# Kernel optimization log

Hardware: AMD Instinct MI355X
Metric: run time of the kernel (lower is better)

Reference implementation:

```python
import jax, jax.numpy as jnp
import numpy as np

NSAMPLE = 16
LEAKY = 0.1


def _leaky(x):
    return jnp.where(x >= 0, x, LEAKY * x)


def _sqdist(src, dst):
    # src [B,N,3], dst [B,M,3] -> [B,N,M]
    d = -2.0 * jnp.einsum('bnc,bmc->bnm', src, dst)
    d = d + jnp.sum(src * src, -1)[:, :, None]
    d = d + jnp.sum(dst * dst, -1)[:, None, :]
    return d


def _knn_idx(query, points, k):
    # query [B,N,3], points [B,M,3] -> [B,N,k] indices of k nearest points
    dist = _sqdist(query, points)
    _, idx = jax.lax.top_k(-dist, k)
    return idx


def _group(points, idx):
    # points [B,M,C], idx [B,N,K] -> [B,N,K,C]
    return jax.vmap(lambda p, i: p[i])(points, idx)


def _cross(xyz1, xyz2, p1, p2, pos_w, pos_b, mlp_params):
    # xyz1 [B,N1,3], xyz2 [B,N2,3], p1 [B,N1,C], p2 [B,N2,C]
    idx = _knn_idx(xyz1, xyz2, NSAMPLE)                       # [B,N1,K]
    neigh_xyz = _group(xyz2, idx)                             # [B,N1,K,3]
    direction = neigh_xyz - xyz1[:, :, None, :]               # [B,N1,K,3]
    g2 = _group(p2, idx)                                      # [B,N1,K,C]
    pos_feat = jnp.einsum('bnkc,oc->bnko', direction, pos_w) + pos_b
    new_pts = _leaky(g2 + p1[:, :, None, :] + pos_feat)       # [B,N1,K,C0]
    for w, b in mlp_params:
        new_pts = _leaky(jnp.einsum('bnkc,oc->bnko', new_pts, w) + b)
    return jnp.max(new_pts, axis=2)                           # [B,N1,Cl]


def setup_inputs() -> dict:
    key = jax.random.key(0)
    ks = jax.random.split(key, 14)
    B, N, D = 2, 8192, 64
    s = 0.1
    return {
        'pc1': jax.random.normal(ks[0], (B, N, 3), jnp.float32),
        'pc2': jax.random.normal(ks[1], (B, N, 3), jnp.float32),
        'feat1': jax.random.normal(ks[2], (B, N, D), jnp.float32),
        'feat2': jax.random.normal(ks[3], (B, N, D), jnp.float32),
        'pos_w': jax.random.normal(ks[4], (64, 3), jnp.float32) * s,
        'pos_b': jax.random.normal(ks[5], (64,), jnp.float32) * s,
        'mlp_w0': jax.random.normal(ks[6], (64, 64), jnp.float32) * s,
        'mlp_b0': jax.random.normal(ks[7], (64,), jnp.float32) * s,
        'mlp_w1': jax.random.normal(ks[8], (64, 64), jnp.float32) * s,
        'mlp_b1': jax.random.normal(ks[9], (64,), jnp.float32) * s,
        't1_w': jax.random.normal(ks[10], (128, 64), jnp.float32) * s,
        't1_b': jax.random.normal(ks[11], (128,), jnp.float32) * s,
        't2_w': jax.random.normal(ks[12], (128, 64), jnp.float32) * s,
        't2_b': jax.random.normal(ks[13], (128,), jnp.float32) * s,
    }


def reference(pc1, pc2, feat1, feat2, pos_w, pos_b, mlp_w0, mlp_b0,
              mlp_w1, mlp_b1, t1_w, t1_b, t2_w, t2_b):
    mlp = [(mlp_w0, mlp_b0), (mlp_w1, mlp_b1)]
    f1 = _cross(pc1, pc2, feat1, feat2, pos_w, pos_b, mlp)    # [B,N1,64]
    f1 = jnp.einsum('bnc,oc->bno', f1, t1_w) + t1_b           # [B,N1,128]
    f2 = _cross(pc2, pc1, feat2, feat1, pos_w, pos_b, mlp)
    f2 = jnp.einsum('bnc,oc->bno', f2, t2_w) + t2_b
    return f1, f2
```

## Files before the change

kernel.cpp:

```cpp
#include <hip/hip_runtime.h>

#define NPTS 8192
#define KNNK 16
#define NSLOT 17
#define LEAKY 0.1f

typedef short bf16x8 __attribute__((ext_vector_type(8)));
typedef float f32x4  __attribute__((ext_vector_type(4)));

#define KTH   1024
#define QPB   128
#define CHN   32
#define GQ    4
#define BUFCAP 48
#define LCAP  6144

__global__ __launch_bounds__(KTH, 4) void knn_kernel(
    const float* __restrict__ pc1, const float* __restrict__ pc2,
    int* __restrict__ knn_out)
{
    __shared__ float sx[NPTS], sy[NPTS], sz[NPTS];
    __shared__ float sbuf[QPB][2 * BUFCAP];
    __shared__ float sthr[QPB];
    __shared__ int   scnt[QPB];
    __shared__ float4 qcoef[QPB];
    __shared__ unsigned short list[LCAP];
    __shared__ int   lcnt;

    const int t   = threadIdx.x;
    const int q0  = blockIdx.x * QPB;
    const int dir = q0 >> 14;
    const int b   = (q0 >> 13) & 1;

    const float* __restrict__ pq    = dir ? pc2 : pc1;
    const float* __restrict__ pcand = dir ? pc1 : pc2;
    const int n0 = q0 & (NPTS - 1);

    const float* src = pcand + (size_t)b * NPTS * 3;
    for (int i = t; i < NPTS; i += KTH) {
        sx[i] = src[3 * i];
        sy[i] = src[3 * i + 1];
        sz[i] = src[3 * i + 2];
    }
    if (t < QPB) {
        scnt[t] = 0;
        const float* qp = pq + ((size_t)b * NPTS + n0 + t) * 3;
        qcoef[t] = make_float4(-2.0f * qp[0], -2.0f * qp[1], -2.0f * qp[2], 0.f);
    }
    if (t == 0) lcnt = 0;
    __syncthreads();

    const int ch = t & (CHN - 1);
    const int qg = t >> 5;

    float q2x[GQ], q2y[GQ], q2z[GQ];
    #pragma unroll
    for (int g = 0; g < GQ; ++g) {
        const float* qp = pq + ((size_t)b * NPTS + n0 + qg * GQ + g) * 3;
        q2x[g] = -2.0f * qp[0];
        q2y[g] = -2.0f * qp[1];
        q2z[g] = -2.0f * qp[2];
    }

    float mA[GQ], mB[GQ];
    #pragma unroll
    for (int g = 0; g < GQ; ++g) { mA[g] = 3.0e38f; mB[g] = 3.0e38f; }

    #pragma unroll 2
    for (int j = 0; j < 32; ++j) {
        const int i0 = j * 128 + 4 * ch;
        const int i1 = i0 + 4096;
        const f32x4 ax = *(const f32x4*)&sx[i0];
        const f32x4 ay = *(const f32x4*)&sy[i0];
        const f32x4 az = *(const f32x4*)&sz[i0];
        const f32x4 bx = *(const f32x4*)&sx[i1];
        const f32x4 by = *(const f32x4*)&sy[i1];
        const f32x4 bz = *(const f32x4*)&sz[i1];
        f32x4 an, bn;
        #pragma unroll
        for (int c = 0; c < 4; ++c) {
            an[c] = fmaf(ax[c], ax[c], fmaf(ay[c], ay[c], az[c] * az[c]));
            bn[c] = fmaf(bx[c], bx[c], fmaf(by[c], by[c], bz[c] * bz[c]));
        }
        #pragma unroll
        for (int g = 0; g < GQ; ++g) {
            #pragma unroll
            for (int c = 0; c < 4; ++c) {
                const float da = fmaf(q2x[g], ax[c],
                                 fmaf(q2y[g], ay[c],
                                 fmaf(q2z[g], az[c], an[c])));
                mA[g] = fminf(mA[g], da);
                const float db = fmaf(q2x[g], bx[c],
                                 fmaf(q2y[g], by[c],
                                 fmaf(q2z[g], bz[c], bn[c])));
                mB[g] = fminf(mB[g], db);
            }
        }
    }

    #pragma unroll
    for (int g = 0; g < GQ; ++g) {
        const int row = qg * GQ + g;
        sbuf[row][ch]      = mA[g];
        sbuf[row][32 + ch] = mB[g];
    }
    __builtin_amdgcn_wave_barrier();

    #pragma unroll
    for (int g = 0; g < GQ; ++g) {
        const int row = qg * GQ + g;
        const float vA = mA[g], vB = mB[g];
        int ltA = 0, eqA = 0, ltB = 0, eqB = 0;
        #pragma unroll
        for (int c = 0; c < 64; c += 2) {
            const float2 vp = *(const float2*)&sbuf[row][c];
            ltA += (vp.x < vA) ? 1 : 0;  eqA += (vp.x == vA) ? 1 : 0;
            ltA += (vp.y < vA) ? 1 : 0;  eqA += (vp.y == vA) ? 1 : 0;
            ltB += (vp.x < vB) ? 1 : 0;  eqB += (vp.x == vB) ? 1 : 0;
            ltB += (vp.y < vB) ? 1 : 0;  eqB += (vp.y == vB) ? 1 : 0;
        }
        if (ltA <= 16 && ltA + eqA > 16) sthr[row] = vA;
        if (ltB <= 16 && ltB + eqB > 16) sthr[row] = vB;
    }
    __syncthreads();

    #pragma unroll
    for (int g = 0; g < GQ; ++g) {
        const int row = qg * GQ + g;
        const float tqv = sthr[row];
        if (mA[g] <= tqv) {
            const int p = atomicAdd(&lcnt, 1);
            if (p < LCAP) list[p] = (unsigned short)((row << 6) | ch);
        }
        if (mB[g] <= tqv) {
            const int p = atomicAdd(&lcnt, 1);
            if (p < LCAP) list[p] = (unsigned short)((row << 6) | 32 | ch);
        }
    }
    __syncthreads();

    {
        const int nsub = min(lcnt, LCAP) * 8;
        for (int k = t; k < nsub; k += KTH) {
            const int e  = list[k >> 3];
            const int s  = k & 7;
            const int q  = e >> 6;
            const int hf = (e >> 5) & 1;
            const int cc = e & 31;
            const float4 qc = qcoef[q];
            const float tqv = sthr[q];
            #pragma unroll
            for (int jj = 0; jj < 4; ++jj) {
                const int i0 = hf * 4096 + (s * 4 + jj) * 128 + 4 * cc;
                const f32x4 cx = *(const f32x4*)&sx[i0];
                const f32x4 cy = *(const f32x4*)&sy[i0];
                const f32x4 cz = *(const f32x4*)&sz[i0];
                #pragma unroll
                for (int c = 0; c < 4; ++c) {
                    const float cn = fmaf(cx[c], cx[c],
                                     fmaf(cy[c], cy[c], cz[c] * cz[c]));
                    const float d  = fmaf(qc.x, cx[c],
                                     fmaf(qc.y, cy[c],
                                     fmaf(qc.z, cz[c], cn)));
                    if (d <= tqv) {
                        const int pos = atomicAdd(&scnt[q], 1);
                        if (pos < BUFCAP) {
                            sbuf[q][pos] = d;
                            ((int*)&sbuf[q][BUFCAP])[pos] = i0 + c;
                        }
                    }
                }
            }
        }
    }
    __syncthreads();

    if (t < QPB) {
        const int nc = min(scnt[t], BUFCAP);

        float dist[NSLOT];
        int   ind[NSLOT];
        #pragma unroll
        for (int i = 0; i < NSLOT; ++i) { dist[i] = 3.0e38f; ind[i] = 0x7fffffff; }

        for (int s = 0; s < nc; ++s) {
            const float d  = sbuf[t][s];
            const int   id = ((int*)&sbuf[t][BUFCAP])[s];
            const bool better0 = (d < dist[0]) || (d == dist[0] && id < ind[0]);
            if (better0) {
                bool cprev = true;
                #pragma unroll
                for (int i = 0; i < NSLOT - 1; ++i) {
                    const bool ci = (d < dist[i + 1]) ||
                                    (d == dist[i + 1] && id < ind[i + 1]);
                    const float nv = ci ? dist[i + 1] : (cprev ? d  : dist[i]);
                    const int   ni = ci ? ind[i + 1]  : (cprev ? id : ind[i]);
                    dist[i] = nv; ind[i] = ni;
                    cprev = ci;
                }
                if (cprev) { dist[NSLOT - 1] = d; ind[NSLOT - 1] = id; }
            }
        }

        const float* qpp = pq + ((size_t)b * NPTS + n0 + t) * 3;
        const double dqx = (double)qpp[0], dqy = (double)qpp[1], dqz = (double)qpp[2];
        double dd[NSLOT];
        #pragma unroll
        for (int i = 0; i < NSLOT; ++i) {
            const int id = ind[i];
            const double dx = (double)sx[id] - dqx;
            const double dy = (double)sy[id] - dqy;
            const double dz = (double)sz[id] - dqz;
            dd[i] = dx * dx + dy * dy + dz * dz;
        }
        int worst = 0; double wd = dd[0];
        #pragma unroll
        for (int i = 1; i < NSLOT; ++i) { if (dd[i] > wd) { wd = dd[i]; worst = i; } }

        int* outp = knn_out + (size_t)(q0 + t) * KNNK;
        int slot = 0;
        #pragma unroll
        for (int i = 0; i < NSLOT; ++i) {
            if (i != worst) outp[slot++] = ind[i];
        }
    }
}

#define PTS 16
#define NG  4

__device__ __forceinline__ unsigned int packhl(float f) {
    const unsigned int u = __float_as_uint(f);
    const unsigned int h = u & 0xffff0000u;
    const float lf = f - __uint_as_float(h);
    return h | (__float_as_uint(lf) >> 16);
}

__device__ __forceinline__ void build_b(const float* __restrict__ wrow,
                                        bf16x8* hi, bf16x8* lo) {
    union { unsigned int u[4]; bf16x8 v; } H, L;
    #pragma unroll
    for (int r = 0; r < 4; ++r) {
        const float f0 = wrow[2 * r], f1 = wrow[2 * r + 1];
        const unsigned int h0 = __float_as_uint(f0) & 0xffff0000u;
        const unsigned int h1 = __float_as_uint(f1) & 0xffff0000u;
        const float l0 = f0 - __uint_as_float(h0);
        const float l1 = f1 - __uint_as_float(h1);
        H.u[r] = h1 | (h0 >> 16);
        L.u[r] = (__float_as_uint(l1) & 0xffff0000u) | (__float_as_uint(l0) >> 16);
    }
    *hi = H.v; *lo = L.v;
}

__device__ __forceinline__ void unpack_a(const unsigned int* __restrict__ Tu,
                                         bf16x8* hi, bf16x8* lo) {
    union { unsigned int u[4]; bf16x8 v; } H, L;
    #pragma unroll
    for (int r = 0; r < 4; ++r) {
        const unsigned int a = Tu[2 * r + 1], bb = Tu[2 * r];
        H.u[r] = __builtin_amdgcn_perm(a, bb, 0x07060302u);
        L.u[r] = __builtin_amdgcn_perm(a, bb, 0x05040100u);
    }
    *hi = H.v; *lo = L.v;
}

__device__ __forceinline__ f32x4 mfma3(f32x4 acc, bf16x8 ah, bf16x8 al,
                                       bf16x8 bh, bf16x8 bl) {
    acc = __builtin_amdgcn_mfma_f32_16x16x32_bf16(ah, bl, acc, 0, 0, 0);
    acc = __builtin_amdgcn_mfma_f32_16x16x32_bf16(al, bh, acc, 0, 0, 0);
    acc = __builtin_amdgcn_mfma_f32_16x16x32_bf16(ah, bh, acc, 0, 0, 0);
    return acc;
}

__global__ __launch_bounds__(256, 4) void feat_kernel(
    const float* __restrict__ pc1, const float* __restrict__ pc2,
    const float* __restrict__ feat1, const float* __restrict__ feat2,
    const float* __restrict__ pos_w, const float* __restrict__ pos_b,
    const float* __restrict__ w0, const float* __restrict__ b0,
    const float* __restrict__ w1, const float* __restrict__ b1,
    const float* __restrict__ t1w, const float* __restrict__ t1b,
    const float* __restrict__ t2w, const float* __restrict__ t2b,
    const int* __restrict__ knn, float* __restrict__ out)
{
    __shared__ unsigned int T0[4][16][68];
    __shared__ unsigned int T1[4][16][68];
    __shared__ float sm[PTS][64];

    const int t    = threadIdx.x;
    const int w    = t >> 6;
    const int lane = t & 63;
    const int m    = lane & 15;
    const int quad = lane >> 4;

    const int p0  = blockIdx.x * PTS;
    const int dir = p0 >> 14, bt = (p0 >> 13) & 1;
    const int n0  = p0 & (NPTS - 1);

    const float* __restrict__ pqd = dir ? pc2 : pc1;
    const float* __restrict__ pcd = dir ? pc1 : pc2;
    const float* __restrict__ fqd = dir ? feat2 : feat1;
    const float* __restrict__ fcd = dir ? feat1 : feat2;

    const int ocol = w * 16 + m;
    bf16x8 Bh[2][2], Bl[2][2];
    #pragma unroll
    for (int kt = 0; kt < 2; ++kt) {
        build_b(&w0[(size_t)ocol * 64 + kt * 32 + quad * 8], &Bh[0][kt], &Bl[0][kt]);
        build_b(&w1[(size_t)ocol * 64 + kt * 32 + quad * 8], &Bh[1][kt], &Bl[1][kt]);
    }
    const float bias1 = b0[ocol];
    const float bias2 = b1[ocol];

    const int cg0 = w * 16 + quad * 4;
    float pbc[4], pwx[4], pwy[4], pwz[4];
    #pragma unroll
    for (int i = 0; i < 4; ++i) {
        pbc[i] = pos_b[cg0 + i];
        pwx[i] = pos_w[(cg0 + i) * 3 + 0];
        pwy[i] = pos_w[(cg0 + i) * 3 + 1];
        pwz[i] = pos_w[(cg0 + i) * 3 + 2];
    }

    float  sdx[4], sdy[4], sdz[4];
    float4 sgf[4], sfq[4];

    auto loadg = [&](int gg) {
        #pragma unroll
        for (int pt = 0; pt < 4; ++pt) {
            const int pp = p0 + gg * 4 + pt;
            const int nn = n0 + gg * 4 + pt;
            const int id = knn[(size_t)pp * KNNK + m];
            const float* qp  = pqd + ((size_t)bt * NPTS + nn) * 3;
            const float* nbp = pcd + ((size_t)bt * NPTS + id) * 3;
            sdx[pt] = nbp[0] - qp[0];
            sdy[pt] = nbp[1] - qp[1];
            sdz[pt] = nbp[2] - qp[2];
            sgf[pt] = *(const float4*)&fcd[((size_t)bt * NPTS + id) * 64 + cg0];
            sfq[pt] = *(const float4*)&fqd[((size_t)bt * NPTS + nn) * 64 + cg0];
        }
    };

    auto storeg = [&]() {
        #pragma unroll
        for (int pt = 0; pt < 4; ++pt) {
            const float gfa[4] = {sgf[pt].x, sgf[pt].y, sgf[pt].z, sgf[pt].w};
            const float fqa[4] = {sfq[pt].x, sfq[pt].y, sfq[pt].z, sfq[pt].w};
            uint4 U;
            unsigned int* Up = (unsigned int*)&U;
            #pragma unroll
            for (int i = 0; i < 4; ++i) {
                float v = gfa[i] + fqa[i] + pbc[i];
                v = fmaf(sdx[pt], pwx[i], v);
                v = fmaf(sdy[pt], pwy[i], v);
                v = fmaf(sdz[pt], pwz[i], v);
                v = fmaxf(v, LEAKY * v);
                Up[i] = packhl(v);
            }
            *(uint4*)&T0[pt][m][cg0] = U;
        }
    };

    loadg(0);
    storeg();
    __syncthreads();

    #pragma unroll
    for (int g = 0; g < NG; ++g) {
        if (g + 1 < NG) loadg(g + 1);

        #pragma unroll
        for (int pt = 0; pt < 4; ++pt) {
            unsigned int Tu[8];
            bf16x8 Ah, Al;
            f32x4 acc = {0.f, 0.f, 0.f, 0.f};
            #pragma unroll
            for (int kt = 0; kt < 2; ++kt) {
                *(uint4*)&Tu[0] = *(const uint4*)&T0[pt][m][kt * 32 + quad * 8];
                *(uint4*)&Tu[4] = *(const uint4*)&T0[pt][m][kt * 32 + quad * 8 + 4];
                unpack_a(Tu, &Ah, &Al);
                acc = mfma3(acc, Ah, Al, Bh[0][kt], Bl[0][kt]);
            }
            #pragma unroll
            for (int r = 0; r < 4; ++r) {
                float v = acc[r] + bias1;
                v = fmaxf(v, LEAKY * v);
                T1[pt][quad * 4 + r][ocol] = packhl(v);
            }
        }
        __syncthreads();

        if (g + 1 < NG) storeg();

        #pragma unroll
        for (int pt = 0; pt < 4; ++pt) {
            unsigned int Tu[8];
            bf16x8 Ah, Al;
            f32x4 acc = {0.f, 0.f, 0.f, 0.f};
            #pragma unroll
            for (int kt = 0; kt < 2; ++kt) {
                *(uint4*)&Tu[0] = *(const uint4*)&T1[pt][m][kt * 32 + quad * 8];
                *(uint4*)&Tu[4] = *(const uint4*)&T1[pt][m][kt * 32 + quad * 8 + 4];
                unpack_a(Tu, &Ah, &Al);
                acc = mfma3(acc, Ah, Al, Bh[1][kt], Bl[1][kt]);
            }
            float mx = -3.0e38f;
            #pragma unroll
            for (int r = 0; r < 4; ++r) {
                float v = acc[r] + bias2;
                v = fmaxf(v, LEAKY * v);
                mx = fmaxf(mx, v);
            }
            mx = fmaxf(mx, __shfl_xor(mx, 16));
            mx = fmaxf(mx, __shfl_xor(mx, 32));
            if (quad == 0) sm[g * 4 + pt][ocol] = mx;
        }
        __syncthreads();
    }

    {
        const float* __restrict__ tw = dir ? t2w : t1w;
        const float* __restrict__ tb = dir ? t2b : t1b;
        const int o  = t & 127;
        const int pg = t >> 7;
        float acc[8];
        const float bz = tb[o];
        #pragma unroll
        for (int i = 0; i < 8; ++i) acc[i] = bz;
        #pragma unroll
        for (int cc = 0; cc < 64; cc += 4) {
            const float4 wq = *(const float4*)&tw[(size_t)o * 64 + cc];
            #pragma unroll
            for (int pr = 0; pr < 4; ++pr) {
                const int pa = (2 * pr + pg) * 2;
                const float4 a0 = *(const float4*)&sm[pa][cc];
                const float4 a1 = *(const float4*)&sm[pa + 1][cc];
                float x0 = acc[2 * pr], x1 = acc[2 * pr + 1];
                x0 = fmaf(a0.x, wq.x, x0); x0 = fmaf(a0.y, wq.y, x0);
                x0 = fmaf(a0.z, wq.z, x0); x0 = fmaf(a0.w, wq.w, x0);
                x1 = fmaf(a1.x, wq.x, x1); x1 = fmaf(a1.y, wq.y, x1);
                x1 = fmaf(a1.z, wq.z, x1); x1 = fmaf(a1.w, wq.w, x1);
                acc[2 * pr] = x0; acc[2 * pr + 1] = x1;
            }
        }
        float* op = out + (size_t)dir * (2 * NPTS * 128);
        #pragma unroll
        for (int pr = 0; pr < 4; ++pr) {
            const int pa = (2 * pr + pg) * 2;
            op[((size_t)bt * NPTS + n0 + pa) * 128 + o]     = acc[2 * pr];
            op[((size_t)bt * NPTS + n0 + pa + 1) * 128 + o] = acc[2 * pr + 1];
        }
    }
}

extern "C" void kernel_launch(void* const* d_in, const int* in_sizes, int n_in,
                              void* d_out, int out_size, void* d_ws, size_t ws_size,
                              hipStream_t stream)
{
    const float* pc1   = (const float*)d_in[0];
    const float* pc2   = (const float*)d_in[1];
    const float* feat1 = (const float*)d_in[2];
    const float* feat2 = (const float*)d_in[3];
    const float* pos_w = (const float*)d_in[4];
    const float* pos_b = (const float*)d_in[5];
    const float* w0    = (const float*)d_in[6];
    const float* b0    = (const float*)d_in[7];
    const float* w1    = (const float*)d_in[8];
    const float* b1    = (const float*)d_in[9];
    const float* t1w   = (const float*)d_in[10];
    const float* t1b   = (const float*)d_in[11];
    const float* t2w   = (const float*)d_in[12];
    const float* t2b   = (const float*)d_in[13];

    int*   knn = (int*)d_ws;
    float* out = (float*)d_out;

    hipLaunchKernelGGL(knn_kernel, dim3(32768 / QPB), dim3(KTH), 0, stream,
                       pc1, pc2, knn);
    hipLaunchKernelGGL(feat_kernel, dim3(32768 / PTS), dim3(256), 0, stream,
                       pc1, pc2, feat1, feat2, pos_w, pos_b,
                       w0, b0, w1, b1, t1w, t1b, t2w, t2b, knn, out);
}
```

Before: 256.5 us.

## Read KNN candidates from a global SoA buffer instead of LDS staging

Adds a prep kernel that converts each candidate point cloud to structure-of-arrays layout in global memory. The KNN kernel then reads candidate coordinates from that buffer instead of copying all 8192 points into shared memory per block. This frees about 96KB of LDS per block, so queries per block are halved and the occupancy hint rises from 4 to 8. The refine pass is re-split into 16 subtasks per list entry. The risk is that the repeated full-candidate scans now go through L2/global memory rather than LDS, and the extra launch adds overhead. If the workspace is too small, d_out is used as scratch, which feat_kernel later overwrites.

```diff
diff --git a/kernel.cpp b/kernel.cpp
--- a/kernel.cpp
+++ b/kernel.cpp
@@ -9,17 +9,32 @@
 typedef float f32x4  __attribute__((ext_vector_type(4)));
 
 #define KTH   1024
-#define QPB   128
+#define QPB   64
 #define CHN   32
-#define GQ    4
+#define GQ    2
 #define BUFCAP 48
-#define LCAP  6144
-
-__global__ __launch_bounds__(KTH, 4) void knn_kernel(
+#define LCAP  3072
+
+
+__global__ __launch_bounds__(256) void prep_kernel(
     const float* __restrict__ pc1, const float* __restrict__ pc2,
-    int* __restrict__ knn_out)
+    float* __restrict__ soa)
 {
-    __shared__ float sx[NPTS], sy[NPTS], sz[NPTS];
+    const int i = blockIdx.x * blockDim.x + threadIdx.x;
+    const int set = i >> 13;
+    const int p   = i & (NPTS - 1);
+    const int dir = set >> 1, b = set & 1;
+    const float* src = (dir ? pc1 : pc2) + ((size_t)b * NPTS + p) * 3;
+    float* dst = soa + (size_t)set * 3 * NPTS;
+    dst[p]            = src[0];
+    dst[NPTS + p]     = src[1];
+    dst[2 * NPTS + p] = src[2];
+}
+
+__global__ __launch_bounds__(KTH, 8) void knn_kernel(
+    const float* __restrict__ pc1, const float* __restrict__ pc2,
+    const float* __restrict__ soa, int* __restrict__ knn_out)
+{
     __shared__ float sbuf[QPB][2 * BUFCAP];
     __shared__ float sthr[QPB];
     __shared__ int   scnt[QPB];
@@ -32,16 +47,12 @@
     const int dir = q0 >> 14;
     const int b   = (q0 >> 13) & 1;
 
-    const float* __restrict__ pq    = dir ? pc2 : pc1;
-    const float* __restrict__ pcand = dir ? pc1 : pc2;
+    const float* __restrict__ pq  = dir ? pc2 : pc1;
+    const float* __restrict__ cxp = soa + (size_t)((dir << 1) | b) * 3 * NPTS;
+    const float* __restrict__ cyp = cxp + NPTS;
+    const float* __restrict__ czp = cxp + 2 * NPTS;
     const int n0 = q0 & (NPTS - 1);
 
-    const float* src = pcand + (size_t)b * NPTS * 3;
-    for (int i = t; i < NPTS; i += KTH) {
-        sx[i] = src[3 * i];
-        sy[i] = src[3 * i + 1];
-        sz[i] = src[3 * i + 2];
-    }
     if (t < QPB) {
         scnt[t] = 0;
         const float* qp = pq + ((size_t)b * NPTS + n0 + t) * 3;
@@ -70,12 +81,12 @@
     for (int j = 0; j < 32; ++j) {
         const int i0 = j * 128 + 4 * ch;
         const int i1 = i0 + 4096;
-        const f32x4 ax = *(const f32x4*)&sx[i0];
-        const f32x4 ay = *(const f32x4*)&sy[i0];
-        const f32x4 az = *(const f32x4*)&sz[i0];
-        const f32x4 bx = *(const f32x4*)&sx[i1];
-        const f32x4 by = *(const f32x4*)&sy[i1];
-        const f32x4 bz = *(const f32x4*)&sz[i1];
+        const f32x4 ax = *(const f32x4*)&cxp[i0];
+        const f32x4 ay = *(const f32x4*)&cyp[i0];
+        const f32x4 az = *(const f32x4*)&czp[i0];
+        const f32x4 bx = *(const f32x4*)&cxp[i1];
+        const f32x4 by = *(const f32x4*)&cyp[i1];
+        const f32x4 bz = *(const f32x4*)&czp[i1];
         f32x4 an, bn;
         #pragma unroll
         for (int c = 0; c < 4; ++c) {
@@ -140,21 +151,22 @@
     __syncthreads();
 
     {
-        const int nsub = min(lcnt, LCAP) * 8;
+        const int nsub = min(lcnt, LCAP) * 16;
         for (int k = t; k < nsub; k += KTH) {
-            const int e  = list[k >> 3];
-            const int s  = k & 7;
+            const int e  = list[k >> 4];
+            const int s  = k & 15;
             const int q  = e >> 6;
             const int hf = (e >> 5) & 1;
             const int cc = e & 31;
             const float4 qc = qcoef[q];
             const float tqv = sthr[q];
             #pragma unroll
-            for (int jj = 0; jj < 4; ++jj) {
-                const int i0 = hf * 4096 + (s * 4 + jj) * 128 + 4 * cc;
-                const f32x4 cx = *(const f32x4*)&sx[i0];
-                const f32x4 cy = *(const f32x4*)&sy[i0];
-                const f32x4 cz = *(const f32x4*)&sz[i0];
+            for (int jj = 0; jj < 2; ++jj) {
+                const int jl = jj * 16 + s;
+                const int i0 = hf * 4096 + jl * 128 + 4 * cc;
+                const f32x4 cx = *(const f32x4*)&cxp[i0];
+                const f32x4 cy = *(const f32x4*)&cyp[i0];
+                const f32x4 cz = *(const f32x4*)&czp[i0];
                 #pragma unroll
                 for (int c = 0; c < 4; ++c) {
                     const float cn = fmaf(cx[c], cx[c],
@@ -208,9 +220,9 @@
         #pragma unroll
         for (int i = 0; i < NSLOT; ++i) {
             const int id = ind[i];
-            const double dx = (double)sx[id] - dqx;
-            const double dy = (double)sy[id] - dqy;
-            const double dz = (double)sz[id] - dqz;
+            const double dx = (double)cxp[id] - dqx;
+            const double dy = (double)cyp[id] - dqy;
+            const double dz = (double)czp[id] - dqz;
             dd[i] = dx * dx + dy * dy + dz * dz;
         }
         int worst = 0; double wd = dd[0];
@@ -474,8 +486,18 @@
     int*   knn = (int*)d_ws;
     float* out = (float*)d_out;
 
+    const size_t knn_bytes = (size_t)32768 * KNNK * sizeof(int);
+    const size_t soa_bytes = (size_t)4 * 3 * NPTS * sizeof(float);
+    float* soa;
+    if (ws_size >= knn_bytes + soa_bytes)
+        soa = (float*)((char*)d_ws + knn_bytes);
+    else
+        soa = (float*)d_out;
+
+    hipLaunchKernelGGL(prep_kernel, dim3(32768 / 256), dim3(256), 0, stream,
+                       pc1, pc2, soa);
     hipLaunchKernelGGL(knn_kernel, dim3(32768 / QPB), dim3(KTH), 0, stream,
-                       pc1, pc2, knn);
+                       pc1, pc2, soa, knn);
     hipLaunchKernelGGL(feat_kernel, dim3(32768 / PTS), dim3(256), 0, stream,
                        pc1, pc2, feat1, feat2, pos_w, pos_b,
                        w0, b0, w1, b1, t1w, t1b, t2w, t2b, knn, out);
```

Result: slower. 345.4 us (+34.6%).
